# Optimization experiments

Measured on AMD Instinct MI355X. Metric: run time of the kernel, lower is better.

## Reference

```python
import jax, jax.numpy as jnp
import numpy as np

PATCH = 256
N = 50000
HC = 256  # height // PATCH
WC = 256  # width // PATCH

def _gauss_kernel():
    # GaussianSmoothing(channels=1, kernel_size=3, sigma=0.5)
    g = np.exp(-(((np.arange(3, dtype=np.float64) - 1.0) / 0.5) ** 2) / 2.0) / (0.5 * np.sqrt(2 * np.pi))
    k = np.outer(g, g)
    k = k / k.sum()
    return jnp.asarray(k, jnp.float32).reshape(1, 1, 3, 3)

def setup_inputs() -> dict:
    key = jax.random.key(0)
    ks = jax.random.split(key, 12)
    h = jax.random.normal(ks[0], (N, 1024), jnp.float32)
    # unique grid cells per patch (row-major), scaled back to pixel coords
    idx = jnp.arange(N, dtype=jnp.int64 if jax.config.jax_enable_x64 else jnp.int32)
    gx = idx % WC
    gy = idx // WC
    coords = jnp.stack([gx * PATCH, gy * PATCH], axis=1)
    eps = jax.random.normal(ks[1], (1, 1, HC, WC), jnp.float32)
    s = 0.02
    W1 = jax.random.normal(ks[2], (512, 1024), jnp.float32) * s
    b1 = jnp.zeros((512,), jnp.float32)
    W2a = jax.random.normal(ks[3], (256, 512), jnp.float32) * s
    b2a = jnp.zeros((256,), jnp.float32)
    W2b = jax.random.normal(ks[4], (256, 512), jnp.float32) * s
    b2b = jnp.zeros((256,), jnp.float32)
    W3 = jax.random.normal(ks[5], (2, 256), jnp.float32) * s
    b3 = jnp.zeros((2,), jnp.float32)
    Wc = jax.random.normal(ks[6], (2, 512), jnp.float32) * s
    bc = jnp.zeros((2,), jnp.float32)
    kernel = _gauss_kernel()
    return {"h": h, "coords": coords, "eps": eps,
            "W1": W1, "b1": b1, "W2a": W2a, "b2a": b2a, "W2b": W2b, "b2b": b2b,
            "W3": W3, "b3": b3, "Wc": Wc, "bc": bc, "kernel": kernel,
            "height": 65536, "width": 65536, "slide_label": 1}

def reference(h, coords, eps, W1, b1, W2a, b2a, W2b, b2b, W3, b3, Wc, bc, kernel, height, width, slide_label):
    hc, wc = height // PATCH, width // PATCH
    x = jax.nn.relu(h @ W1.T + b1)                      # [N,512] (dropout = eval identity)
    fa = jax.nn.sigmoid(x @ W2a.T + b2a)                # [N,256]
    fb = jnp.tanh(x @ W2b.T + b2b)                      # [N,256]
    params = (fa * fb) @ W3.T + b3                      # [N,2] -> (mu, logvar) per patch
    gx = coords[:, 0] // PATCH
    gy = coords[:, 1] // PATCH
    mu = jnp.zeros((1, hc, wc), x.dtype).at[0, gy, gx].set(params[:, 0])
    logvar = jnp.zeros((1, hc, wc), x.dtype).at[0, gy, gx].set(params[:, 1])
    prior_mu = jnp.array([-5.0, 0.0], x.dtype)[slide_label]
    prior_lv = jnp.array([-1.0, 3.0], x.dtype)[slide_label]
    kl_div = (prior_lv - logvar) / 2.0 + (logvar ** 2 + (prior_mu - mu) ** 2) / (2.0 * prior_lv ** 2) - 0.5
    mu_pad = jnp.pad(mu, ((0, 0), (1, 1), (1, 1)))[None]          # [1,1,hc+2,wc+2]
    mu_sm = jax.lax.conv_general_dilated(mu_pad, kernel, (1, 1), 'VALID')  # [1,1,hc,wc]
    samples = mu_sm + eps * jnp.exp(0.5 * logvar)                  # reparameterize, broadcast to [1,1,hc,wc]
    A = jax.nn.sigmoid(samples[0])                                 # [1,hc,wc]
    patch_A = A[0, gy, gx][None]                                   # gather -> [1,N]
    M = (patch_A @ x) / patch_A.sum()                              # [1,512]
    logits = M @ Wc.T + bc                                         # [1,n_classes]
    y_probs = jax.nn.softmax(logits, axis=1)
    top_idx = jax.lax.top_k(y_probs[:, 1], 1)[1]                   # top_k=1
    top_instance = logits[top_idx]                                 # [1,n_classes]
    Y_hat = jnp.argmax(top_instance, axis=1, keepdims=True)
    Y_prob = jax.nn.softmax(top_instance, axis=1)
    return (top_instance, Y_prob, Y_hat, kl_div, y_probs, patch_A)
```

## Files before the change

kernel.cpp:

```cpp
#include <hip/hip_runtime.h>
#include <hip/hip_bf16.h>
#include <cstdint>
#include <cstddef>

#define NPATCH 50000
#define GC 256

typedef __bf16 bf16x8 __attribute__((ext_vector_type(8)));
typedef float  f32x4  __attribute__((ext_vector_type(4)));
typedef float  f32x8  __attribute__((ext_vector_type(8)));

static constexpr size_t XB_OFF    = 0;
static constexpr size_t XB_BYTES  = (size_t)50048 * 512 * 2;
static constexpr size_t W1B_OFF   = XB_OFF + XB_BYTES;
static constexpr size_t W1B_BYTES = (size_t)512 * 1024 * 2;
static constexpr size_t W2AB_OFF  = W1B_OFF + W1B_BYTES;
static constexpr size_t W2X_BYTES = (size_t)256 * 512 * 2;
static constexpr size_t W2BB_OFF  = W2AB_OFF + W2X_BYTES;
static constexpr size_t MUG_OFF   = W2BB_OFF + W2X_BYTES;
static constexpr size_t LVG_OFF   = MUG_OFF + (size_t)65536 * 4;
static constexpr size_t AG_OFF    = LVG_OFF + (size_t)65536 * 4;
static constexpr size_t MPART_OFF = AG_OFF + (size_t)65536 * 4;
static constexpr size_t SUMA_OFF  = MPART_OFF + (size_t)512 * 4;
static constexpr size_t ZERO_BYTES = SUMA_OFF + 4 - MUG_OFF;

__device__ __forceinline__ unsigned short f2bf(float f) {
  union { float f; uint32_t u; } v; v.f = f;
  uint32_t u = v.u;
  uint32_t r = (u + 0x7FFFu + ((u >> 16) & 1u)) >> 16;
  return (unsigned short)r;
}
__device__ __forceinline__ float bf2f(uint32_t bits16) {
  union { uint32_t u; float f; } v; v.u = bits16 << 16; return v.f;
}
__device__ __forceinline__ unsigned short cvt_bf16(float f) {
  __bf16 b = (__bf16)f;
  return __builtin_bit_cast(unsigned short, b);
}
__device__ __forceinline__ void gld16(const void* g, void* l) {
  __builtin_amdgcn_global_load_lds(
      (const __attribute__((address_space(1))) void*)g,
      (__attribute__((address_space(3))) void*)l, 16, 0, 0);
}

__global__ void convert_weights(const float* __restrict__ W1,
                                const float* __restrict__ W2a,
                                const float* __restrict__ W2b,
                                unsigned short* __restrict__ W1b,
                                unsigned short* __restrict__ W2ab,
                                unsigned short* __restrict__ W2bb) {
  int i = blockIdx.x * 256 + threadIdx.x;
  if (i < 512 * 1024) W1b[i] = f2bf(W1[i]);
  if (i < 256 * 512) { W2ab[i] = f2bf(W2a[i]); W2bb[i] = f2bf(W2b[i]); }
}

#define G1_BM 128
#define G1_BK 32

__global__ __launch_bounds__(512, 2) void gemm1(
    const float* __restrict__ h, const unsigned short* __restrict__ W1b,
    const float* __restrict__ b1, unsigned short* __restrict__ xb) {
  __shared__ __align__(16) unsigned short As[2][G1_BM * G1_BK];
  __shared__ __align__(16) unsigned short Bs[2][512 * G1_BK];

  const int t  = threadIdx.x;
  const int l  = t & 63;
  const int w  = t >> 6;
  const int wr = w >> 2;
  const int wc = w & 3;
  const int g  = l >> 4;
  const int lr = l & 15;
  const int rowBase = blockIdx.x * G1_BM;

  const int arow  = t >> 2;
  const int ablk  = t & 3;
  const int agrow = rowBase + arow;
  const bool aval = agrow < NPATCH;
  const float* asrc = h + (size_t)agrow * 1024 + ablk * 8;
  const int awoff = arow * G1_BK + ablk * 8;

  const unsigned short* bsrc[4];
  int bdst[4];
#pragma unroll
  for (int q = 0; q < 4; ++q) {
    int c = w * 4 + q;
    int rowb = c * 16 + (l >> 2);
    bsrc[q] = W1b + (size_t)rowb * 1024 + (l & 3) * 8;
    bdst[q] = c * 16 * G1_BK;
  }

  f32x4 acc[4][8];
#pragma unroll
  for (int m = 0; m < 4; ++m)
#pragma unroll
    for (int n = 0; n < 8; ++n) acc[m][n] = (f32x4){0.f, 0.f, 0.f, 0.f};

  {
    float4 f0 = {0.f,0.f,0.f,0.f}, f1 = {0.f,0.f,0.f,0.f};
    if (aval) {
      f0 = *(const float4*)(asrc + 0);
      f1 = *(const float4*)(asrc + 4);
    }
#pragma unroll
    for (int q = 0; q < 4; ++q) gld16(bsrc[q], &Bs[0][bdst[q]]);
    f32x8 fv;
    fv[0]=f0.x; fv[1]=f0.y; fv[2]=f0.z; fv[3]=f0.w;
    fv[4]=f1.x; fv[5]=f1.y; fv[6]=f1.z; fv[7]=f1.w;
    bf16x8 bv = __builtin_convertvector(fv, bf16x8);
    *(bf16x8*)&As[0][awoff] = bv;
  }
  __syncthreads();

  int cur = 0;
  for (int kt = 0; kt < 32; ++kt) {
    const bool pf = kt < 31;
    float4 f0 = {0.f,0.f,0.f,0.f}, f1 = {0.f,0.f,0.f,0.f};
    if (pf) {
      if (aval) {
        f0 = *(const float4*)(asrc + (kt + 1) * G1_BK);
        f1 = *(const float4*)(asrc + (kt + 1) * G1_BK + 4);
      }
      const int nxt = cur ^ 1;
#pragma unroll
      for (int q = 0; q < 4; ++q)
        gld16(bsrc[q] + (size_t)(kt + 1) * G1_BK, &Bs[nxt][bdst[q]]);
    }
    bf16x8 af[4], bfr[8];
#pragma unroll
    for (int m = 0; m < 4; ++m)
      af[m] = *(const bf16x8*)&As[cur][(wr * 64 + m * 16 + lr) * G1_BK + g * 8];
#pragma unroll
    for (int n = 0; n < 8; ++n)
      bfr[n] = *(const bf16x8*)&Bs[cur][(wc * 128 + n * 16 + lr) * G1_BK + g * 8];
#pragma unroll
    for (int m = 0; m < 4; ++m)
#pragma unroll
      for (int n = 0; n < 8; ++n)
        acc[m][n] = __builtin_amdgcn_mfma_f32_16x16x32_bf16(af[m], bfr[n], acc[m][n], 0, 0, 0);
    if (pf) {
      f32x8 fv;
      fv[0]=f0.x; fv[1]=f0.y; fv[2]=f0.z; fv[3]=f0.w;
      fv[4]=f1.x; fv[5]=f1.y; fv[6]=f1.z; fv[7]=f1.w;
      bf16x8 bv = __builtin_convertvector(fv, bf16x8);
      *(bf16x8*)&As[cur ^ 1][awoff] = bv;
    }
    __syncthreads();
    cur ^= 1;
  }

  float b1v[8];
#pragma unroll
  for (int n = 0; n < 8; ++n) b1v[n] = b1[wc * 128 + n * 16 + lr];
#pragma unroll
  for (int m = 0; m < 4; ++m) {
    const int rb0 = rowBase + wr * 64 + m * 16 + g * 4;
#pragma unroll
    for (int r = 0; r < 4; ++r) {
      const int row = rb0 + r;
      if (row < NPATCH) {
        unsigned short* xrow = xb + (size_t)row * 512 + wc * 128;
#pragma unroll
        for (int n = 0; n < 8; ++n) {
          float v = acc[m][n][r] + b1v[n];
          v = v > 0.f ? v : 0.f;
          xrow[n * 16 + lr] = cvt_bf16(v);
        }
      }
    }
  }
}

__global__ __launch_bounds__(256, 2) void gemm2(
    const unsigned short* __restrict__ xb,
    const unsigned short* __restrict__ W2ab, const unsigned short* __restrict__ W2bb,
    const float* __restrict__ b2a, const float* __restrict__ b2b,
    const float* __restrict__ W3, const float* __restrict__ b3,
    const int* __restrict__ coords,
    float* __restrict__ mug, float* __restrict__ lvg) {
  __shared__ __align__(16) unsigned short xs[64 * 40];
  __shared__ __align__(16) unsigned short was[256 * 40];
  __shared__ __align__(16) unsigned short wbs[256 * 40];
  __shared__ float pmu_s[4][64];
  __shared__ float plv_s[4][64];

  const int t = threadIdx.x;
  const int l = t & 63;
  const int w = t >> 6;
  const int g = l >> 4, lr = l & 15;
  const int rowBase = blockIdx.x * 64;

  f32x4 aa[4][4], ab[4][4];
#pragma unroll
  for (int m = 0; m < 4; ++m)
#pragma unroll
    for (int n = 0; n < 4; ++n) {
      aa[m][n] = (f32x4){0.f, 0.f, 0.f, 0.f};
      ab[m][n] = (f32x4){0.f, 0.f, 0.f, 0.f};
    }

  const int xrow = t >> 2;
  const int xc0  = (t & 3) * 8;
  const int grow = rowBase + xrow;
  const bool xval = grow < NPATCH;

  for (int kt = 0; kt < 16; ++kt) {
    const int k0 = kt * 32;
    __syncthreads();
    if (xval) {
      *(int4*)&xs[xrow * 40 + xc0] = *(const int4*)(xb + (size_t)grow * 512 + k0 + xc0);
    } else {
      int4 z = {0, 0, 0, 0};
      *(int4*)&xs[xrow * 40 + xc0] = z;
    }
#pragma unroll
    for (int j = 0; j < 4; ++j) {
      int rrow = (t >> 2) + 64 * j;
      *(int4*)&was[rrow * 40 + xc0] = *(const int4*)(W2ab + (size_t)rrow * 512 + k0 + xc0);
      *(int4*)&wbs[rrow * 40 + xc0] = *(const int4*)(W2bb + (size_t)rrow * 512 + k0 + xc0);
    }
    __syncthreads();

    bf16x8 af[4], ba[4], bb[4];
#pragma unroll
    for (int m = 0; m < 4; ++m)
      af[m] = *(const bf16x8*)&xs[(m * 16 + lr) * 40 + g * 8];
#pragma unroll
    for (int n = 0; n < 4; ++n) {
      int brow = w * 64 + n * 16 + lr;
      ba[n] = *(const bf16x8*)&was[brow * 40 + g * 8];
      bb[n] = *(const bf16x8*)&wbs[brow * 40 + g * 8];
    }
#pragma unroll
    for (int m = 0; m < 4; ++m)
#pragma unroll
      for (int n = 0; n < 4; ++n) {
        aa[m][n] = __builtin_amdgcn_mfma_f32_16x16x32_bf16(af[m], ba[n], aa[m][n], 0, 0, 0);
        ab[m][n] = __builtin_amdgcn_mfma_f32_16x16x32_bf16(af[m], bb[n], ab[m][n], 0, 0, 0);
      }
  }

  float b2av[4], b2bv[4], w30v[4], w31v[4];
#pragma unroll
  for (int n = 0; n < 4; ++n) {
    int col = w * 64 + n * 16 + lr;
    b2av[n] = b2a[col]; b2bv[n] = b2b[col];
    w30v[n] = W3[col];  w31v[n] = W3[256 + col];
  }
#pragma unroll
  for (int m = 0; m < 4; ++m) {
#pragma unroll
    for (int r = 0; r < 4; ++r) {
      float pm = 0.f, pl = 0.f;
#pragma unroll
      for (int n = 0; n < 4; ++n) {
        float a = 1.f / (1.f + __expf(-(aa[m][n][r] + b2av[n])));
        float b = tanhf(ab[m][n][r] + b2bv[n]);
        float p = a * b;
        pm += p * w30v[n];
        pl += p * w31v[n];
      }
#pragma unroll
      for (int d = 1; d < 16; d <<= 1) {
        pm += __shfl_xor(pm, d, 64);
        pl += __shfl_xor(pl, d, 64);
      }
      if (lr == 0) {
        pmu_s[w][m * 16 + g * 4 + r] = pm;
        plv_s[w][m * 16 + g * 4 + r] = pl;
      }
    }
  }
  __syncthreads();
  if (t < 64) {
    float mu = pmu_s[0][t] + pmu_s[1][t] + pmu_s[2][t] + pmu_s[3][t] + b3[0];
    float lv = plv_s[0][t] + plv_s[1][t] + plv_s[2][t] + plv_s[3][t] + b3[1];
    int row = rowBase + t;
    if (row < NPATCH) {
      int gx = coords[2 * row] >> 8;
      int gy = coords[2 * row + 1] >> 8;
      int cell = gy * GC + gx;
      mug[cell] = mu;
      lvg[cell] = lv;
    }
  }
}

__global__ void grid_ops(const float* __restrict__ mug, const float* __restrict__ lvg,
                         const float* __restrict__ eps, const float* __restrict__ kern,
                         const int* __restrict__ slide, float* __restrict__ Ag,
                         float* __restrict__ out_kl) {
  int cell = blockIdx.x * 256 + threadIdx.x;
  int iy = cell >> 8, ix = cell & 255;
  float mu = mug[cell], lv = lvg[cell];
  int sl = slide[0];
  float pm  = (sl == 0) ? -5.0f : 0.0f;
  float plv = (sl == 0) ? -1.0f : 3.0f;
  float d = pm - mu;
  out_kl[cell] = (plv - lv) * 0.5f + (lv * lv + d * d) / (2.0f * plv * plv) - 0.5f;
  float s = 0.f;
#pragma unroll
  for (int dy = 0; dy < 3; ++dy) {
#pragma unroll
    for (int dx = 0; dx < 3; ++dx) {
      int y = iy + dy - 1, x = ix + dx - 1;
      if (y >= 0 && y < GC && x >= 0 && x < GC)
        s += mug[y * GC + x] * kern[dy * 3 + dx];
    }
  }
  float sample = s + eps[cell] * __expf(0.5f * lv);
  Ag[cell] = 1.f / (1.f + __expf(-sample));
}

__global__ __launch_bounds__(256) void patch_pass(
    const float* __restrict__ Ag, const int* __restrict__ coords,
    const unsigned short* __restrict__ xb, float* __restrict__ out_pA,
    float* __restrict__ Mpart, float* __restrict__ sumA) {
  __shared__ float als[256];
  __shared__ float swave[4];
  const int t = threadIdx.x;
  const int base = blockIdx.x * 256;
  const int row = base + t;
  float a = 0.f;
  if (row < NPATCH) {
    int gx = coords[2 * row] >> 8;
    int gy = coords[2 * row + 1] >> 8;
    a = Ag[gy * GC + gx];
    out_pA[row] = a;
  }
  als[t] = a;
  float sa = a;
#pragma unroll
  for (int d = 1; d < 64; d <<= 1) sa += __shfl_xor(sa, d, 64);
  if ((t & 63) == 0) swave[t >> 6] = sa;
  __syncthreads();
  if (t == 0) atomicAdd(sumA, swave[0] + swave[1] + swave[2] + swave[3]);

  const int nrows = min(256, NPATCH - base);
  float m0 = 0.f, m1 = 0.f;
  for (int r = 0; r < nrows; ++r) {
    float av = als[r];
    const uint32_t* p = (const uint32_t*)(xb + (size_t)(base + r) * 512);
    uint32_t v = p[t];
    m0 += av * bf2f(v & 0xFFFFu);
    m1 += av * bf2f(v >> 16);
  }
  atomicAdd(&Mpart[t * 2 + 0], m0);
  atomicAdd(&Mpart[t * 2 + 1], m1);
}

__global__ void finalize(const float* __restrict__ Mpart, const float* __restrict__ sumA,
                         const float* __restrict__ Wc, const float* __restrict__ bc,
                         float* __restrict__ out) {
  const int t = threadIdx.x;
  float s = sumA[0];
  float l0 = 0.f, l1 = 0.f;
#pragma unroll
  for (int j = 0; j < 8; ++j) {
    int c = t * 8 + j;
    float m = Mpart[c] / s;
    l0 += m * Wc[c];
    l1 += m * Wc[512 + c];
  }
#pragma unroll
  for (int d = 1; d < 64; d <<= 1) {
    l0 += __shfl_xor(l0, d, 64);
    l1 += __shfl_xor(l1, d, 64);
  }
  if (t == 0) {
    l0 += bc[0]; l1 += bc[1];
    float mx = fmaxf(l0, l1);
    float e0 = __expf(l0 - mx), e1 = __expf(l1 - mx);
    float inv = 1.f / (e0 + e1);
    float p0 = e0 * inv, p1 = e1 * inv;
    out[0] = l0; out[1] = l1;
    out[2] = p0; out[3] = p1;
    out[4] = (l1 > l0) ? 1.0f : 0.0f;
    out[65541] = p0; out[65542] = p1;
  }
}

extern "C" void kernel_launch(void* const* d_in, const int* in_sizes, int n_in,
                              void* d_out, int out_size, void* d_ws, size_t ws_size,
                              hipStream_t stream) {
  const float* h      = (const float*)d_in[0];
  const int*   coords = (const int*)d_in[1];
  const float* eps    = (const float*)d_in[2];
  const float* W1     = (const float*)d_in[3];
  const float* b1     = (const float*)d_in[4];
  const float* W2a    = (const float*)d_in[5];
  const float* b2a    = (const float*)d_in[6];
  const float* W2b    = (const float*)d_in[7];
  const float* b2b    = (const float*)d_in[8];
  const float* W3     = (const float*)d_in[9];
  const float* b3     = (const float*)d_in[10];
  const float* Wc     = (const float*)d_in[11];
  const float* bc     = (const float*)d_in[12];
  const float* kern   = (const float*)d_in[13];
  const int*   slide  = (const int*)d_in[16];
  float* out = (float*)d_out;
  char*  ws  = (char*)d_ws;

  unsigned short* xb   = (unsigned short*)(ws + XB_OFF);
  unsigned short* W1b  = (unsigned short*)(ws + W1B_OFF);
  unsigned short* W2ab = (unsigned short*)(ws + W2AB_OFF);
  unsigned short* W2bb = (unsigned short*)(ws + W2BB_OFF);
  float* mug   = (float*)(ws + MUG_OFF);
  float* lvg   = (float*)(ws + LVG_OFF);
  float* Ag    = (float*)(ws + AG_OFF);
  float* Mpart = (float*)(ws + MPART_OFF);
  float* sumA  = (float*)(ws + SUMA_OFF);

  hipMemsetAsync(ws + MUG_OFF, 0, ZERO_BYTES, stream);

  convert_weights<<<2048, 256, 0, stream>>>(W1, W2a, W2b, W1b, W2ab, W2bb);
  gemm1<<<391, 512, 0, stream>>>(h, W1b, b1, xb);
  gemm2<<<782, 256, 0, stream>>>(xb, W2ab, W2bb, b2a, b2b, W3, b3, coords, mug, lvg);
  grid_ops<<<256, 256, 0, stream>>>(mug, lvg, eps, kern, slide, Ag, out + 5);
  patch_pass<<<196, 256, 0, stream>>>(Ag, coords, xb, out + 65543, Mpart, sumA);
  finalize<<<1, 64, 0, stream>>>(Mpart, sumA, Wc, bc, out);
}
```

Before: 221.2 us.

## Retile gemm1 to 64x256 blocks with direct-from-global B fragments and swizzled A

gemm1 now uses 256-thread blocks, each computing a 64-row by 256-column tile on a 2x782 grid, instead of 128x512 tiles over 391 blocks. The W1 tile is no longer staged in LDS: each wave loads its bf16 B fragments straight from global memory (the weights should stay cached) and only the converted h tile goes through LDS, with an XOR swizzle to avoid bank conflicts. The h prefetch is now issued two k-steps ahead, and the smaller LDS and register footprint allow more blocks per CU. In exchange, every h row tile is read and converted twice (once per column half), and the B operand is fetched through the cache rather than shared in LDS.

```diff
diff --git a/kernel.cpp b/kernel.cpp
--- a/kernel.cpp
+++ b/kernel.cpp
@@ -37,11 +37,6 @@
   __bf16 b = (__bf16)f;
   return __builtin_bit_cast(unsigned short, b);
 }
-__device__ __forceinline__ void gld16(const void* g, void* l) {
-  __builtin_amdgcn_global_load_lds(
-      (const __attribute__((address_space(1))) void*)g,
-      (__attribute__((address_space(3))) void*)l, 16, 0, 0);
-}
 
 __global__ void convert_weights(const float* __restrict__ W1,
                                 const float* __restrict__ W2a,
@@ -54,113 +49,99 @@
   if (i < 256 * 512) { W2ab[i] = f2bf(W2a[i]); W2bb[i] = f2bf(W2b[i]); }
 }
 
-#define G1_BM 128
-#define G1_BK 32
-
-__global__ __launch_bounds__(512, 2) void gemm1(
+__global__ __launch_bounds__(256, 4) void gemm1(
     const float* __restrict__ h, const unsigned short* __restrict__ W1b,
     const float* __restrict__ b1, unsigned short* __restrict__ xb) {
-  __shared__ __align__(16) unsigned short As[2][G1_BM * G1_BK];
-  __shared__ __align__(16) unsigned short Bs[2][512 * G1_BK];
+  __shared__ __align__(16) unsigned short As[2][64 * 32];
 
   const int t  = threadIdx.x;
   const int l  = t & 63;
-  const int w  = t >> 6;
-  const int wr = w >> 2;
-  const int wc = w & 3;
+  const int wc = t >> 6;
   const int g  = l >> 4;
   const int lr = l & 15;
-  const int rowBase = blockIdx.x * G1_BM;
+  const int rowBase = blockIdx.y * 64;
+  const int colBase = blockIdx.x * 256;
 
   const int arow  = t >> 2;
   const int ablk  = t & 3;
   const int agrow = rowBase + arow;
   const bool aval = agrow < NPATCH;
   const float* asrc = h + (size_t)agrow * 1024 + ablk * 8;
-  const int awoff = arow * G1_BK + ablk * 8;
-
-  const unsigned short* bsrc[4];
-  int bdst[4];
-#pragma unroll
-  for (int q = 0; q < 4; ++q) {
-    int c = w * 4 + q;
-    int rowb = c * 16 + (l >> 2);
-    bsrc[q] = W1b + (size_t)rowb * 1024 + (l & 3) * 8;
-    bdst[q] = c * 16 * G1_BK;
-  }
-
-  f32x4 acc[4][8];
+  const int awoff = arow * 32 + ((ablk ^ ((arow >> 1) & 3)) * 8);
+
+  const unsigned short* bptr[4];
+#pragma unroll
+  for (int n = 0; n < 4; ++n)
+    bptr[n] = W1b + (size_t)(colBase + wc * 64 + n * 16 + lr) * 1024 + g * 8;
+
+  int aroff[4];
+#pragma unroll
+  for (int m = 0; m < 4; ++m) {
+    int ra = m * 16 + lr;
+    aroff[m] = ra * 32 + ((g ^ ((ra >> 1) & 3)) * 8);
+  }
+
+  f32x4 acc[4][4];
 #pragma unroll
   for (int m = 0; m < 4; ++m)
 #pragma unroll
-    for (int n = 0; n < 8; ++n) acc[m][n] = (f32x4){0.f, 0.f, 0.f, 0.f};
-
+    for (int n = 0; n < 4; ++n) acc[m][n] = (f32x4){0.f, 0.f, 0.f, 0.f};
+
+  float4 a0 = {0.f,0.f,0.f,0.f}, a1 = {0.f,0.f,0.f,0.f};
   {
-    float4 f0 = {0.f,0.f,0.f,0.f}, f1 = {0.f,0.f,0.f,0.f};
-    if (aval) {
-      f0 = *(const float4*)(asrc + 0);
-      f1 = *(const float4*)(asrc + 4);
-    }
-#pragma unroll
-    for (int q = 0; q < 4; ++q) gld16(bsrc[q], &Bs[0][bdst[q]]);
+    if (aval) { a0 = *(const float4*)(asrc + 0); a1 = *(const float4*)(asrc + 4); }
     f32x8 fv;
-    fv[0]=f0.x; fv[1]=f0.y; fv[2]=f0.z; fv[3]=f0.w;
-    fv[4]=f1.x; fv[5]=f1.y; fv[6]=f1.z; fv[7]=f1.w;
-    bf16x8 bv = __builtin_convertvector(fv, bf16x8);
-    *(bf16x8*)&As[0][awoff] = bv;
+    fv[0]=a0.x; fv[1]=a0.y; fv[2]=a0.z; fv[3]=a0.w;
+    fv[4]=a1.x; fv[5]=a1.y; fv[6]=a1.z; fv[7]=a1.w;
+    *(bf16x8*)&As[0][awoff] = __builtin_convertvector(fv, bf16x8);
+    a0 = (float4){0.f,0.f,0.f,0.f}; a1 = a0;
+    if (aval) { a0 = *(const float4*)(asrc + 32); a1 = *(const float4*)(asrc + 36); }
   }
   __syncthreads();
 
   int cur = 0;
   for (int kt = 0; kt < 32; ++kt) {
-    const bool pf = kt < 31;
-    float4 f0 = {0.f,0.f,0.f,0.f}, f1 = {0.f,0.f,0.f,0.f};
-    if (pf) {
+    if (kt < 31) {
+      f32x8 fv;
+      fv[0]=a0.x; fv[1]=a0.y; fv[2]=a0.z; fv[3]=a0.w;
+      fv[4]=a1.x; fv[5]=a1.y; fv[6]=a1.z; fv[7]=a1.w;
+      *(bf16x8*)&As[cur ^ 1][awoff] = __builtin_convertvector(fv, bf16x8);
+    }
+    if (kt < 30) {
+      a0 = (float4){0.f,0.f,0.f,0.f}; a1 = a0;
       if (aval) {
-        f0 = *(const float4*)(asrc + (kt + 1) * G1_BK);
-        f1 = *(const float4*)(asrc + (kt + 1) * G1_BK + 4);
-      }
-      const int nxt = cur ^ 1;
-#pragma unroll
-      for (int q = 0; q < 4; ++q)
-        gld16(bsrc[q] + (size_t)(kt + 1) * G1_BK, &Bs[nxt][bdst[q]]);
-    }
-    bf16x8 af[4], bfr[8];
-#pragma unroll
-    for (int m = 0; m < 4; ++m)
-      af[m] = *(const bf16x8*)&As[cur][(wr * 64 + m * 16 + lr) * G1_BK + g * 8];
-#pragma unroll
-    for (int n = 0; n < 8; ++n)
-      bfr[n] = *(const bf16x8*)&Bs[cur][(wc * 128 + n * 16 + lr) * G1_BK + g * 8];
-#pragma unroll
-    for (int m = 0; m < 4; ++m)
-#pragma unroll
-      for (int n = 0; n < 8; ++n)
-        acc[m][n] = __builtin_amdgcn_mfma_f32_16x16x32_bf16(af[m], bfr[n], acc[m][n], 0, 0, 0);
-    if (pf) {
-      f32x8 fv;
-      fv[0]=f0.x; fv[1]=f0.y; fv[2]=f0.z; fv[3]=f0.w;
-      fv[4]=f1.x; fv[5]=f1.y; fv[6]=f1.z; fv[7]=f1.w;
-      bf16x8 bv = __builtin_convertvector(fv, bf16x8);
-      *(bf16x8*)&As[cur ^ 1][awoff] = bv;
+        a0 = *(const float4*)(asrc + (kt + 2) * 32);
+        a1 = *(const float4*)(asrc + (kt + 2) * 32 + 4);
+      }
+    }
+    bf16x8 bfr[4];
+#pragma unroll
+    for (int n = 0; n < 4; ++n)
+      bfr[n] = *(const bf16x8*)(bptr[n] + kt * 32);
+#pragma unroll
+    for (int m = 0; m < 4; ++m) {
+      bf16x8 af = *(const bf16x8*)&As[cur][aroff[m]];
+#pragma unroll
+      for (int n = 0; n < 4; ++n)
+        acc[m][n] = __builtin_amdgcn_mfma_f32_16x16x32_bf16(af, bfr[n], acc[m][n], 0, 0, 0);
     }
     __syncthreads();
     cur ^= 1;
   }
 
-  float b1v[8];
-#pragma unroll
-  for (int n = 0; n < 8; ++n) b1v[n] = b1[wc * 128 + n * 16 + lr];
+  float b1v[4];
+#pragma unroll
+  for (int n = 0; n < 4; ++n) b1v[n] = b1[colBase + wc * 64 + n * 16 + lr];
 #pragma unroll
   for (int m = 0; m < 4; ++m) {
-    const int rb0 = rowBase + wr * 64 + m * 16 + g * 4;
+    const int rb0 = rowBase + m * 16 + g * 4;
 #pragma unroll
     for (int r = 0; r < 4; ++r) {
       const int row = rb0 + r;
       if (row < NPATCH) {
-        unsigned short* xrow = xb + (size_t)row * 512 + wc * 128;
-#pragma unroll
-        for (int n = 0; n < 8; ++n) {
+        unsigned short* xrow = xb + (size_t)row * 512 + colBase + wc * 64;
+#pragma unroll
+        for (int n = 0; n < 4; ++n) {
           float v = acc[m][n][r] + b1v[n];
           v = v > 0.f ? v : 0.f;
           xrow[n * 16 + lr] = cvt_bf16(v);
@@ -413,7 +394,7 @@
   hipMemsetAsync(ws + MUG_OFF, 0, ZERO_BYTES, stream);
 
   convert_weights<<<2048, 256, 0, stream>>>(W1, W2a, W2b, W1b, W2ab, W2bb);
-  gemm1<<<391, 512, 0, stream>>>(h, W1b, b1, xb);
+  gemm1<<<dim3(2, 782), 256, 0, stream>>>(h, W1b, b1, xb);
   gemm2<<<782, 256, 0, stream>>>(xb, W2ab, W2bb, b2a, b2b, W3, b3, coords, mug, lvg);
   grid_ops<<<256, 256, 0, stream>>>(mug, lvg, eps, kern, slide, Ag, out + 5);
   patch_pass<<<196, 256, 0, stream>>>(Ag, coords, xb, out + 65543, Mpart, sumA);
```

Result: slower. 249.5 us (+12.8%).
